# Kernel tuning notes

Measured on AMD Instinct MI355X. Metric: run time of the kernel, lower is better.

The kernel has to match this reference:

```python
import jax, jax.numpy as jnp
import numpy as np

ITER_STEPS = 2


def setup_inputs() -> dict:
    key = jax.random.key(0)
    ks = jax.random.split(key, 9)
    B, N, D, E = 64, 256, 512, 10  # batch, nodes, node_dim, edge types
    node = jax.random.normal(ks[0], (B, N, D), dtype=jnp.float32)
    node_mask = jax.random.randint(ks[1], (B, N), 0, 2).astype(jnp.int32)
    adj = jax.random.randint(ks[2], (E, B, N, N), 0, 2).astype(jnp.int32)
    s = 0.02
    W_nw = jax.random.normal(ks[3], (1, D), dtype=jnp.float32) * s   # node weight fc [out=1, in=D]
    b_nw = jnp.zeros((1,), dtype=jnp.float32)
    W_self = jax.random.normal(ks[4], (D, D), dtype=jnp.float32) * s
    b_self = jnp.zeros((D,), dtype=jnp.float32)
    W_edge = jax.random.normal(ks[5], (E, D, D), dtype=jnp.float32) * s  # per-edge-type Linear (no bias)
    return {"node": node, "W_nw": W_nw, "b_nw": b_nw, "W_self": W_self,
            "b_self": b_self, "W_edge": W_edge, "node_mask": node_mask, "adj": adj}


def reference(node, W_nw, b_nw, W_self, b_self, W_edge, node_mask, adj):
    # node: [B,N,D]; node_mask: [B,N] int; adj: [E=10,B,N,N] int (binary)
    B, N, D = node.shape
    m = node_mask.astype(node.dtype)
    eye = jnp.eye(N, dtype=node.dtype)
    # dd_graph = mask outer-product with zeroed diagonal: [B,N,N]
    dd = m[:, None, :] * m[:, :, None] * (1.0 - eye)
    graphs = dd[None] * adj.astype(node.dtype)  # [E,B,N,N]
    # total neighbor count across all 10 edge types, clamped to >=1 (replace_masked_values)
    neigh = graphs.sum(axis=(0, 3))                       # [B,N]
    neigh = jnp.where(neigh >= 1.0, neigh, 1.0)
    all_weight = []
    for _ in range(ITER_STEPS):
        # (1) node relatedness gate
        w = jax.nn.sigmoid(node @ W_nw.T + b_nw)[..., 0]  # [B,N]
        all_weight.append(w)
        self_info = node @ W_self.T + b_self              # [B,N,D]
        # (2) per-edge-type projection + masked adjacency matmul, summed over edge types
        proj = jnp.einsum('bnk,edk->ebnd', node, W_edge)  # [E,B,N,D]
        masked_w = jnp.where(graphs != 0, w[None, :, None, :], 0.0)  # [E,B,N,N]
        agg = jnp.einsum('ebnm,ebmd->bnd', masked_w, proj)           # [B,N,D]
        # (3) update
        node = jax.nn.relu(self_info + agg / neigh[..., None])
    return node, jnp.stack(all_weight, axis=1)  # ([B,N,D], [B,ITER,N])
```

## Files before the change

kernel.cpp:

```cpp
#include <hip/hip_runtime.h>
#include <hip/hip_bf16.h>

#define BB 64
#define NN 256
#define DD 512
#define EE 10

typedef __bf16 bf16x8 __attribute__((ext_vector_type(8)));
typedef unsigned short ushort8v __attribute__((ext_vector_type(8)));
typedef unsigned int uint4v __attribute__((ext_vector_type(4)));
typedef unsigned int uint2v __attribute__((ext_vector_type(2)));
typedef float floatx4 __attribute__((ext_vector_type(4)));
typedef float floatx16 __attribute__((ext_vector_type(16)));

typedef __attribute__((address_space(3))) unsigned short lds_us;
typedef const __attribute__((address_space(1))) unsigned short glb_us;

__device__ __forceinline__ unsigned short f2b(float f) {
    union { float f; unsigned u; } x; x.f = f;
    unsigned r = x.u + 0x7FFFu + ((x.u >> 16) & 1u);
    return (unsigned short)(r >> 16);
}
__device__ __forceinline__ float b2f(unsigned short u) {
    union { unsigned u; float f; } x; x.u = ((unsigned)u) << 16;
    return x.f;
}
__device__ __forceinline__ unsigned pack_bf16(float a, float b) {
    union { float f; unsigned u; } xa, xb2; xa.f = a; xb2.f = b;
    return __builtin_amdgcn_perm(xa.u + 0x8000u, xb2.u + 0x8000u, 0x07060302u);
}
__device__ __forceinline__ bf16x8 frag_from_nibs(unsigned n0, unsigned n1) {
    unsigned r80a = n0 << 7, r80b = n1 << 7;
    unsigned r3fa = n0 * 63u, r3fb = n1 * 63u;
    uint4v av;
    av[0] = __builtin_amdgcn_perm(r3fa, r80a, 0x05010400u);
    av[1] = __builtin_amdgcn_perm(r3fa, r80a, 0x07030602u);
    av[2] = __builtin_amdgcn_perm(r3fb, r80b, 0x05010400u);
    av[3] = __builtin_amdgcn_perm(r3fb, r80b, 0x07030602u);
    return __builtin_bit_cast(bf16x8, av);
}

__global__ void k_wconv(const float* __restrict__ W_edge,
                        const float* __restrict__ W_self,
                        unsigned short* __restrict__ Wf) {
    int t = blockIdx.x * 256 + threadIdx.x;
    int lane  = t & 63;
    int kstep = (t >> 6) & 31;
    int cfg   = (t >> 11) & 15;
    int e     = t >> 15;
    int dout = cfg * 32 + (lane & 31);
    int k    = kstep * 16 + (lane >> 5) * 8;
    const float* src = (e < EE) ? (W_edge + ((size_t)e * DD + dout) * DD + k)
                                : (W_self + (size_t)dout * DD + k);
    ushort8v o;
    #pragma unroll
    for (int j = 0; j < 8; j++) o[j] = f2b(src[j]);
    *(ushort8v*)(Wf + (size_t)t * 8) = o;
}

__global__ void k_graph(const int* __restrict__ adj, const int* __restrict__ mask,
                        unsigned* __restrict__ packed, float* __restrict__ recip) {
    int b = blockIdx.x >> 8;
    int n = blockIdx.x & 255;
    int lane = threadIdx.x & 63;
    int wv   = threadIdx.x >> 6;
    int m = wv * 64 + lane;
    int ok = (mask[b * NN + n] != 0) & (mask[b * NN + m] != 0) & (m != n);
    __shared__ int cnt_s[4];
    int total = 0;
    #pragma unroll
    for (int e = 0; e < EE; e++) {
        int a = adj[(((size_t)e * BB + b) * NN + n) * NN + m];
        int bit = ok & (a != 0);
        unsigned long long bal = __ballot(bit);
        if (lane == 0) {
            unsigned* dst = packed + (((size_t)e * BB + b) * NN + n) * 8 + wv * 2;
            dst[0] = (unsigned)bal;
            dst[1] = (unsigned)(bal >> 32);
        }
        total += bit;
    }
    for (int off = 32; off; off >>= 1) total += __shfl_down(total, off);
    if (lane == 0) cnt_s[wv] = total;
    __syncthreads();
    if (threadIdx.x == 0) {
        int c = cnt_s[0] + cnt_s[1] + cnt_s[2] + cnt_s[3];
        recip[b * NN + n] = 1.0f / (float)(c < 1 ? 1 : c);
    }
}

template<int TI>
__global__ __launch_bounds__(256)
void k_gt(const float* __restrict__ xf, const unsigned short* __restrict__ xbin,
          const float* __restrict__ W_nw, const float* __restrict__ b_nw,
          float* __restrict__ w_out, unsigned short* __restrict__ wTf,
          unsigned short* __restrict__ xb0) {
    int bid = blockIdx.x;
    int b  = bid >> 4;
    int ms = bid & 15;
    __shared__ float part[16][17];
    __shared__ float wsig[16];
    int t = threadIdx.x;
    int row = t >> 4;
    int seg = t & 15;
    size_t g = ((size_t)(b * NN + ms * 16 + row)) * DD + seg * 32;
    float s = 0.f;
    if (TI == 0) {
        const floatx4* xp = (const floatx4*)(xf + g);
        const floatx4* wp = (const floatx4*)(W_nw + seg * 32);
        #pragma unroll
        for (int k = 0; k < 4; k++) {
            floatx4 a = xp[2 * k], c4 = xp[2 * k + 1];
            floatx4 wa = wp[2 * k], wc = wp[2 * k + 1];
            ushort8v u;
            #pragma unroll
            for (int j = 0; j < 4; j++) {
                s += a[j] * wa[j] + c4[j] * wc[j];
                u[j] = f2b(a[j]); u[4 + j] = f2b(c4[j]);
            }
            *(ushort8v*)(xb0 + g + k * 8) = u;
        }
    } else {
        const ushort8v* xp = (const ushort8v*)(xbin + g);
        const float* wp = W_nw + seg * 32;
        #pragma unroll
        for (int k = 0; k < 4; k++) {
            ushort8v u = xp[k];
            #pragma unroll
            for (int j = 0; j < 8; j++) s += b2f(u[j]) * wp[k * 8 + j];
        }
    }
    part[row][seg] = s;
    __syncthreads();
    if (t < 16) {
        float tot = 0.f;
        #pragma unroll
        for (int i = 0; i < 16; i++) tot += part[t][i];
        float v = 1.f / (1.f + __expf(-(tot + b_nw[0])));
        wsig[t] = v;
        w_out[(b * 2 + TI) * NN + ms * 16 + t] = v;
    }
    __syncthreads();
    #pragma unroll
    for (int c = 0; c < 4; c++) {
        int slot = t + 256 * c;
        int dd_  = slot >> 6;
        int lane = slot & 63;
        int l31 = lane & 31, hi = lane >> 5;
        size_t xrow = ((size_t)(b * NN + ms * 16 + hi * 8)) * DD + dd_ * 32 + l31;
        ushort8v o;
        #pragma unroll
        for (int j = 0; j < 8; j++) {
            float xv = (TI == 0) ? xf[xrow + (size_t)j * DD] : b2f(xbin[xrow + (size_t)j * DD]);
            o[j] = f2b(xv * wsig[hi * 8 + j]);
        }
        *(ushort8v*)(wTf + ((((size_t)b * 16 + ms) * 16 + dd_) * 64 + lane) * 8) = o;
    }
}

template<int TI>
__global__ __launch_bounds__(512, 4)
void k2_heavy(const unsigned short* __restrict__ wTf,
              const unsigned short* __restrict__ xb,
              const unsigned short* __restrict__ Wf,
              const unsigned* __restrict__ packed,
              const float* __restrict__ recip,
              const float* __restrict__ b_self,
              unsigned short* __restrict__ out_bf16,
              float* __restrict__ out_f32) {
    __shared__ __attribute__((aligned(16))) unsigned short sWT[64 * 512];
    __shared__ __attribute__((aligned(16))) unsigned short sTf[16 * 512];

    int bid = blockIdx.x;
    int ct = bid & 1;
    int b  = (bid >> 1) & 63;
    int nq = bid >> 7;
    int w = threadIdx.x >> 6, lane = threadIdx.x & 63;
    int l31 = lane & 31, hi = lane >> 5;

    int s1_d = w >> 1, s1_nb = w & 1;
    int gn1 = nq * 64 + s1_nb * 32 + l31;

    floatx16 acc2[2];
    #pragma unroll
    for (int i = 0; i < 2; i++)
        #pragma unroll
        for (int q = 0; q < 16; q++) acc2[i][q] = 0.f;

    auto stage_sWT = [&](int dc2) {
        #pragma unroll
        for (int it = 0; it < 8; it++) {
            int c = it * 8 + w;
            const unsigned short* g = wTf +
                ((((size_t)b * 16 + (c >> 2)) * 16 + dc2 * 4 + (c & 3)) * 64 + lane) * 8;
            __builtin_amdgcn_global_load_lds((glb_us*)g, (lds_us*)&sWT[c * 512], 16, 0, 0);
        }
    };

    stage_sWT(0);

    const unsigned short* WfL = Wf + lane * 8;
    const unsigned short* xbL = xb + ((size_t)(b * NN + nq * 64 + l31)) * DD + hi * 8;

    unsigned bq[32];

    #pragma unroll 1
    for (int s = 0; s < 40; s++) {
        int e = s >> 2, dc2 = s & 3;
        asm volatile("s_waitcnt vmcnt(0) lgkmcnt(0)" ::: "memory");
        __builtin_amdgcn_s_barrier();
        if ((s & 3) == 0) {
            const uint4v* pp = (const uint4v*)(packed +
                (((size_t)e * BB + b) * NN + gn1) * 8);
            uint4v pa = pp[0], pbv = pp[1];
            unsigned pwv[8] = {pa[0], pa[1], pa[2], pa[3], pbv[0], pbv[1], pbv[2], pbv[3]};
            #pragma unroll
            for (int ks = 0; ks < 8; ks++) {
                unsigned byA = (pwv[ks] >> (hi * 8)) & 0xFFu;
                unsigned byB = (pwv[ks] >> ((2 + hi) * 8)) & 0xFFu;
                bq[ks * 4 + 0] = ((byA & 0xFu) * 0x00204081u) & 0x01010101u;
                bq[ks * 4 + 1] = (((byA >> 4) & 0xFu) * 0x00204081u) & 0x01010101u;
                bq[ks * 4 + 2] = ((byB & 0xFu) * 0x00204081u) & 0x01010101u;
                bq[ks * 4 + 3] = (((byB >> 4) & 0xFu) * 0x00204081u) & 0x01010101u;
            }
        }
        {
            floatx16 acc3;
            #pragma unroll
            for (int q = 0; q < 16; q++) acc3[q] = 0.f;
            #pragma unroll
            for (int mk = 0; mk < 16; mk++) {
                bf16x8 afr = __builtin_bit_cast(bf16x8,
                    *(const ushort8v*)&sWT[(mk * 4 + s1_d) * 512 + lane * 8]);
                bf16x8 bg = frag_from_nibs(bq[(mk >> 1) * 4 + (mk & 1) * 2],
                                           bq[(mk >> 1) * 4 + (mk & 1) * 2 + 1]);
                acc3 = __builtin_amdgcn_mfma_f32_32x32x16_bf16(afr, bg, acc3, 0, 0, 0);
            }
            #pragma unroll
            for (int g = 0; g < 4; g++) {
                uint2v pk;
                pk[0] = pack_bf16(acc3[g * 4 + 1], acc3[g * 4 + 0]);
                pk[1] = pack_bf16(acc3[g * 4 + 3], acc3[g * 4 + 2]);
                int kk_w = s1_d * 2 + (g >> 1);
                int slot = (kk_w * 2 + s1_nb) * 64 + (g & 1) * 32 + l31;
                *(uint2v*)&sTf[slot * 8 + 4 * hi] = pk;
            }
        }
        asm volatile("s_waitcnt lgkmcnt(0)" ::: "memory");
        __builtin_amdgcn_s_barrier();
        if (s + 1 < 40) stage_sWT((s + 1) & 3);
        #pragma unroll
        for (int kk = 0; kk < 8; kk++) {
            bf16x8 bfr = __builtin_bit_cast(bf16x8, *(const ushort8v*)
                &WfL[(size_t)(((e * 16 + ct * 8 + w) * 32 + dc2 * 8 + kk)) * 512]);
            bf16x8 afr0 = __builtin_bit_cast(bf16x8,
                *(const ushort8v*)&sTf[((kk * 2 + 0) * 64 + lane) * 8]);
            bf16x8 afr1 = __builtin_bit_cast(bf16x8,
                *(const ushort8v*)&sTf[((kk * 2 + 1) * 64 + lane) * 8]);
            acc2[0] = __builtin_amdgcn_mfma_f32_32x32x16_bf16(afr0, bfr, acc2[0], 0, 0, 0);
            acc2[1] = __builtin_amdgcn_mfma_f32_32x32x16_bf16(afr1, bfr, acc2[1], 0, 0, 0);
        }
    }
    #pragma unroll
    for (int nb = 0; nb < 2; nb++) {
        #pragma unroll
        for (int rg = 0; rg < 16; rg++) {
            int row = nq * 64 + nb * 32 + (rg & 3) + 8 * (rg >> 2) + 4 * hi;
            acc2[nb][rg] *= recip[b * NN + row];
        }
    }
    #pragma unroll 1
    for (int dc2 = 0; dc2 < 4; dc2++) {
        #pragma unroll
        for (int kk = 0; kk < 8; kk++) {
            bf16x8 bfr = __builtin_bit_cast(bf16x8, *(const ushort8v*)
                &WfL[(size_t)(((EE * 16 + ct * 8 + w) * 32 + dc2 * 8 + kk)) * 512]);
            bf16x8 afr0 = __builtin_bit_cast(bf16x8, *(const ushort8v*)
                &xbL[(size_t)0 * 32 * DD + (dc2 * 8 + kk) * 16]);
            bf16x8 afr1 = __builtin_bit_cast(bf16x8, *(const ushort8v*)
                &xbL[(size_t)1 * 32 * DD + (dc2 * 8 + kk) * 16]);
            acc2[0] = __builtin_amdgcn_mfma_f32_32x32x16_bf16(afr0, bfr, acc2[0], 0, 0, 0);
            acc2[1] = __builtin_amdgcn_mfma_f32_32x32x16_bf16(afr1, bfr, acc2[1], 0, 0, 0);
        }
    }
    {
        int col = ct * 256 + w * 32 + l31;
        float bs = b_self[col];
        #pragma unroll
        for (int nb = 0; nb < 2; nb++) {
            #pragma unroll
            for (int rg = 0; rg < 16; rg++) {
                int row = nq * 64 + nb * 32 + (rg & 3) + 8 * (rg >> 2) + 4 * hi;
                float v = acc2[nb][rg] + bs;
                v = v > 0.f ? v : 0.f;
                size_t gi = ((size_t)b * NN + row) * DD + col;
                if (TI == 0) out_bf16[gi] = f2b(v);
                else         out_f32[gi] = v;
            }
        }
    }
}

extern "C" void kernel_launch(void* const* d_in, const int* in_sizes, int n_in,
                              void* d_out, int out_size, void* d_ws, size_t ws_size,
                              hipStream_t stream) {
    const float* node   = (const float*)d_in[0];
    const float* W_nw   = (const float*)d_in[1];
    const float* b_nw   = (const float*)d_in[2];
    const float* W_self = (const float*)d_in[3];
    const float* b_self = (const float*)d_in[4];
    const float* W_edge = (const float*)d_in[5];
    const int*   mask   = (const int*)d_in[6];
    const int*   adj    = (const int*)d_in[7];
    float* out = (float*)d_out;
    float* out_w = out + (size_t)BB * NN * DD;

    char* ws = (char*)d_ws;
    size_t off = 0;
    unsigned short* Wf    = (unsigned short*)(ws + off); off += (size_t)11 * DD * DD * 2;
    unsigned short* wTf   = (unsigned short*)(ws + off); off += (size_t)BB * DD * NN * 2;
    unsigned short* xb0   = (unsigned short*)(ws + off); off += (size_t)BB * NN * DD * 2;
    unsigned short* xb1   = (unsigned short*)(ws + off); off += (size_t)BB * NN * DD * 2;
    unsigned*       packed= (unsigned*)(ws + off);       off += (size_t)EE * BB * NN * 8 * 4;
    float*          recip = (float*)(ws + off);          off += (size_t)BB * NN * 4;

    k_wconv<<<dim3(1408), dim3(256), 0, stream>>>(W_edge, W_self, Wf);
    k_graph<<<dim3(16384), dim3(256), 0, stream>>>(adj, mask, packed, recip);

    k_gt<0><<<dim3(1024), dim3(256), 0, stream>>>(node, nullptr, W_nw, b_nw, out_w, wTf, xb0);
    k2_heavy<0><<<dim3(512), dim3(512), 0, stream>>>(wTf, xb0, Wf, packed, recip, b_self, xb1, nullptr);

    k_gt<1><<<dim3(1024), dim3(256), 0, stream>>>(nullptr, xb1, W_nw, b_nw, out_w, wTf, nullptr);
    k2_heavy<1><<<dim3(512), dim3(512), 0, stream>>>(wTf, xb1, Wf, packed, recip, b_self, nullptr, out);
}
```

Before: 721.6 us.

## Read wTf fragments directly from global and double-buffer sTf to drop a barrier

Removes the LDS staging buffer for the weighted-transposed node tile (sWT) and its async global_load_lds prefetch. Each wave now reads its MFMA A-fragments straight from global memory (L2/L1). sTf is double-buffered by iteration parity, which allows the barrier at the top of each step to be dropped. This cuts LDS footprint (raising possible occupancy) and one barrier per step. In exchange it exposes global-load latency inside the inner MFMA loop and gives up the overlap the prefetch provided. The diff also adds a redundant, oddly computed bq write that is immediately overwritten.

```diff
diff --git a/kernel.cpp b/kernel.cpp
--- a/kernel.cpp
+++ b/kernel.cpp
@@ -12,9 +12,6 @@
 typedef unsigned int uint2v __attribute__((ext_vector_type(2)));
 typedef float floatx4 __attribute__((ext_vector_type(4)));
 typedef float floatx16 __attribute__((ext_vector_type(16)));
-
-typedef __attribute__((address_space(3))) unsigned short lds_us;
-typedef const __attribute__((address_space(1))) unsigned short glb_us;
 
 __device__ __forceinline__ unsigned short f2b(float f) {
     union { float f; unsigned u; } x; x.f = f;
@@ -168,8 +165,7 @@
               const float* __restrict__ b_self,
               unsigned short* __restrict__ out_bf16,
               float* __restrict__ out_f32) {
-    __shared__ __attribute__((aligned(16))) unsigned short sWT[64 * 512];
-    __shared__ __attribute__((aligned(16))) unsigned short sTf[16 * 512];
+    __shared__ __attribute__((aligned(16))) unsigned short sTf[2][16 * 512];
 
     int bid = blockIdx.x;
     int ct = bid & 1;
@@ -187,28 +183,15 @@
         #pragma unroll
         for (int q = 0; q < 16; q++) acc2[i][q] = 0.f;
 
-    auto stage_sWT = [&](int dc2) {
-        #pragma unroll
-        for (int it = 0; it < 8; it++) {
-            int c = it * 8 + w;
-            const unsigned short* g = wTf +
-                ((((size_t)b * 16 + (c >> 2)) * 16 + dc2 * 4 + (c & 3)) * 64 + lane) * 8;
-            __builtin_amdgcn_global_load_lds((glb_us*)g, (lds_us*)&sWT[c * 512], 16, 0, 0);
-        }
-    };
-
-    stage_sWT(0);
-
     const unsigned short* WfL = Wf + lane * 8;
     const unsigned short* xbL = xb + ((size_t)(b * NN + nq * 64 + l31)) * DD + hi * 8;
+    const unsigned short* wTfA = wTf + ((size_t)b * 256 + s1_d) * 512 + lane * 8;
 
     unsigned bq[32];
 
     #pragma unroll 1
     for (int s = 0; s < 40; s++) {
-        int e = s >> 2, dc2 = s & 3;
-        asm volatile("s_waitcnt vmcnt(0) lgkmcnt(0)" ::: "memory");
-        __builtin_amdgcn_s_barrier();
+        int e = s >> 2, dc2 = s & 3, cur = s & 1;
         if ((s & 3) == 0) {
             const uint4v* pp = (const uint4v*)(packed +
                 (((size_t)e * BB + b) * NN + gn1) * 8);
@@ -221,6 +204,11 @@
                 bq[ks * 4 + 0] = ((byA & 0xFu) * 0x00204081u) & 0x01010101u;
                 bq[ks * 4 + 1] = (((byA >> 4) & 0xFu) * 0x00204081u) & 0x01010101u;
                 bq[ks * 4 + 2] = ((byB & 0xFu) * 0x00204081u) & 0x01010101u;
+                bq[ks * 4 + 3] = (((byB >> 4) & 0xFu) * 0x01010101u & 0x01010101u);
+            }
+            #pragma unroll
+            for (int ks = 0; ks < 8; ks++) {
+                unsigned byB = (pwv[ks] >> ((2 + hi) * 8)) & 0xFFu;
                 bq[ks * 4 + 3] = (((byB >> 4) & 0xFu) * 0x00204081u) & 0x01010101u;
             }
         }
@@ -231,7 +219,7 @@
             #pragma unroll
             for (int mk = 0; mk < 16; mk++) {
                 bf16x8 afr = __builtin_bit_cast(bf16x8,
-                    *(const ushort8v*)&sWT[(mk * 4 + s1_d) * 512 + lane * 8]);
+                    *(const ushort8v*)&wTfA[(size_t)(mk * 16 + dc2 * 4) * 512]);
                 bf16x8 bg = frag_from_nibs(bq[(mk >> 1) * 4 + (mk & 1) * 2],
                                            bq[(mk >> 1) * 4 + (mk & 1) * 2 + 1]);
                 acc3 = __builtin_amdgcn_mfma_f32_32x32x16_bf16(afr, bg, acc3, 0, 0, 0);
@@ -243,20 +231,19 @@
                 pk[1] = pack_bf16(acc3[g * 4 + 3], acc3[g * 4 + 2]);
                 int kk_w = s1_d * 2 + (g >> 1);
                 int slot = (kk_w * 2 + s1_nb) * 64 + (g & 1) * 32 + l31;
-                *(uint2v*)&sTf[slot * 8 + 4 * hi] = pk;
+                *(uint2v*)&sTf[cur][slot * 8 + 4 * hi] = pk;
             }
         }
         asm volatile("s_waitcnt lgkmcnt(0)" ::: "memory");
         __builtin_amdgcn_s_barrier();
-        if (s + 1 < 40) stage_sWT((s + 1) & 3);
         #pragma unroll
         for (int kk = 0; kk < 8; kk++) {
             bf16x8 bfr = __builtin_bit_cast(bf16x8, *(const ushort8v*)
                 &WfL[(size_t)(((e * 16 + ct * 8 + w) * 32 + dc2 * 8 + kk)) * 512]);
             bf16x8 afr0 = __builtin_bit_cast(bf16x8,
-                *(const ushort8v*)&sTf[((kk * 2 + 0) * 64 + lane) * 8]);
+                *(const ushort8v*)&sTf[cur][((kk * 2 + 0) * 64 + lane) * 8]);
             bf16x8 afr1 = __builtin_bit_cast(bf16x8,
-                *(const ushort8v*)&sTf[((kk * 2 + 1) * 64 + lane) * 8]);
+                *(const ushort8v*)&sTf[cur][((kk * 2 + 1) * 64 + lane) * 8]);
             acc2[0] = __builtin_amdgcn_mfma_f32_32x32x16_bf16(afr0, bfr, acc2[0], 0, 0, 0);
             acc2[1] = __builtin_amdgcn_mfma_f32_32x32x16_bf16(afr1, bfr, acc2[1], 0, 0, 0);
         }
```

New measurement: 739.4 us. 1.02x slower.
